# Optimization experiments

Measured on AMD Instinct MI355X. Metric: run time of the kernel, lower is better.

Reference implementation:

```python
import jax, jax.numpy as jnp
import numpy as np

N_BINS = 15
N, C = 1000000, 128


def setup_inputs() -> dict:
    key = jax.random.key(0)
    k1, k2 = jax.random.split(key)
    logits = jax.random.normal(k1, (N, C), dtype=jnp.float32)
    labels = jax.random.randint(k2, (N,), 0, C, dtype=jnp.int32)
    return {"logits": logits, "labels": labels}


def reference(logits, labels):
    # softmax + confidence/prediction (single pass, no [N,C] score re-materialization beyond probs)
    probs = jax.nn.softmax(logits, axis=1)            # [N, C]
    conf = jnp.max(probs, axis=1)                     # [N]
    pred = jnp.argmax(probs, axis=1)                  # [N]
    acc = (pred == labels).astype(conf.dtype)         # [N]

    # bin i covers (i/n_bins, (i+1)/n_bins]; searchsorted(uppers, conf, 'left')
    # gives the smallest j with uppers[j] >= conf, i.e. conf <= upper and conf > lower
    uppers = jnp.linspace(0.0, 1.0, N_BINS + 1, dtype=conf.dtype)[1:]  # [n_bins]
    bin_idx = jnp.clip(jnp.searchsorted(uppers, conf, side="left"), 0, N_BINS - 1)

    # fused histogram / segment reduce replacing the per-bin python loop
    counts = jax.ops.segment_sum(jnp.ones_like(conf), bin_idx, num_segments=N_BINS)
    sum_conf = jax.ops.segment_sum(conf, bin_idx, num_segments=N_BINS)
    sum_acc = jax.ops.segment_sum(acc, bin_idx, num_segments=N_BINS)

    nonempty = counts > 0
    safe = jnp.where(nonempty, counts, jnp.ones_like(counts))
    avg_conf = sum_conf / safe                        # per-bin avg confidence
    avg_acc = sum_acc / safe                          # per-bin accuracy

    gap = jnp.abs(avg_conf - avg_acc)
    # max over non-empty bins only (original skips bins with prop_in_bin == 0)
    mce = jnp.max(jnp.where(nonempty, gap, -jnp.inf))

    prob = jnp.where(nonempty, avg_conf, jnp.zeros_like(avg_conf))
    accu = jnp.where(nonempty, avg_acc, jnp.zeros_like(avg_acc))
    return mce, prob, accu
```

## Files before the change

### kernel.cpp

```cpp
#include <hip/hip_runtime.h>

#define NBINS 15

__global__ __launch_bounds__(256) void mce_pass1(
    const float* __restrict__ logits, const int* __restrict__ labels,
    unsigned long long* __restrict__ conf_part,
    unsigned int* __restrict__ cnt_part,
    unsigned int* __restrict__ acc_part,
    int n)
{
    __shared__ unsigned int s_cnt[NBINS];
    __shared__ unsigned int s_acc[NBINS];
    __shared__ unsigned long long s_conf[NBINS];
    if (threadIdx.x < NBINS) {
        s_cnt[threadIdx.x] = 0u;
        s_acc[threadIdx.x] = 0u;
        s_conf[threadIdx.x] = 0ULL;
    }
    __syncthreads();

    const int lane32 = threadIdx.x & 31;
    const int half   = (threadIdx.x >> 5) & 1;
    const int hw_global = blockIdx.x * 8 + (threadIdx.x >> 5);
    const int hw_total = gridDim.x * 8;

    for (int row = hw_global; row < n; row += hw_total) {
        const float4 v = *(const float4*)(logits + (size_t)row * 128 + lane32 * 4);
        const int lab = labels[row];

        float m4 = fmaxf(fmaxf(v.x, v.y), fmaxf(v.z, v.w));

        float M = m4;
        #pragma unroll
        for (int off = 16; off >= 1; off >>= 1)
            M = fmaxf(M, __shfl_xor(M, off, 32));

        int idx_local = (v.x == M) ? 0 : (v.y == M) ? 1 : (v.z == M) ? 2 : 3;
        unsigned long long bal = __ballot(m4 == M);
        unsigned int mask32 = (unsigned int)(bal >> (half << 5));
        int win_lane = __ffs(mask32) - 1;
        int win_local = __shfl(idx_local, win_lane, 32);
        int pred = (win_lane << 2) + win_local;

        float s = __expf(v.x - M) + __expf(v.y - M) + __expf(v.z - M) + __expf(v.w - M);
        #pragma unroll
        for (int off = 16; off >= 1; off >>= 1)
            s += __shfl_xor(s, off, 32);

        if (lane32 == 0) {
            float conf = 1.0f / s;
            int bin = (int)ceilf(conf * 15.0f) - 1;
            bin = max(0, min(NBINS - 1, bin));
            unsigned int acc = (pred == lab) ? 1u : 0u;
            unsigned long long fc = (unsigned long long)((double)conf * 4294967296.0);
            atomicAdd(&s_cnt[bin], 1u);
            atomicAdd(&s_acc[bin], acc);
            atomicAdd(&s_conf[bin], fc);
        }
    }
    __syncthreads();
    if (threadIdx.x < NBINS) {
        cnt_part[blockIdx.x * NBINS + threadIdx.x]  = s_cnt[threadIdx.x];
        acc_part[blockIdx.x * NBINS + threadIdx.x]  = s_acc[threadIdx.x];
        conf_part[blockIdx.x * NBINS + threadIdx.x] = s_conf[threadIdx.x];
    }
}

__global__ __launch_bounds__(960) void mce_pass2(
    const unsigned long long* __restrict__ conf_part,
    const unsigned int* __restrict__ cnt_part,
    const unsigned int* __restrict__ acc_part,
    int B, float* __restrict__ out)
{
    __shared__ float s_prob[NBINS], s_accu[NBINS], s_gap[NBINS];
    __shared__ int s_ne[NBINS];

    const int bin  = threadIdx.x >> 6;
    const int lane = threadIdx.x & 63;

    unsigned long long csum = 0ULL;
    unsigned int cn = 0u, ac = 0u;
    for (int i = lane; i < B; i += 64) {
        csum += conf_part[i * NBINS + bin];
        cn   += cnt_part[i * NBINS + bin];
        ac   += acc_part[i * NBINS + bin];
    }
    #pragma unroll
    for (int off = 32; off >= 1; off >>= 1) {
        csum += __shfl_xor(csum, off, 64);
        cn   += __shfl_xor(cn, off, 64);
        ac   += __shfl_xor(ac, off, 64);
    }

    if (lane == 0) {
        if (cn > 0u) {
            float p = (float)(((double)csum * (1.0 / 4294967296.0)) / (double)cn);
            float a = (float)((double)ac / (double)cn);
            s_prob[bin] = p;
            s_accu[bin] = a;
            s_gap[bin]  = fabsf(p - a);
            s_ne[bin]   = 1;
        } else {
            s_prob[bin] = 0.0f;
            s_accu[bin] = 0.0f;
            s_gap[bin]  = 0.0f;
            s_ne[bin]   = 0;
        }
    }
    __syncthreads();

    if (threadIdx.x == 0) {
        float mce = -1e30f;
        for (int b = 0; b < NBINS; ++b)
            if (s_ne[b] && s_gap[b] > mce) mce = s_gap[b];
        out[0] = mce;
    }
    if (threadIdx.x < NBINS) {
        out[1 + threadIdx.x]  = s_prob[threadIdx.x];
        out[16 + threadIdx.x] = s_accu[threadIdx.x];
    }
}

extern "C" void kernel_launch(void* const* d_in, const int* in_sizes, int n_in,
                              void* d_out, int out_size, void* d_ws, size_t ws_size,
                              hipStream_t stream) {
    const float* logits = (const float*)d_in[0];
    const int*   labels = (const int*)d_in[1];
    const int n = in_sizes[1];

    int B = 2048;
    const size_t per_block = (size_t)NBINS * (8 + 4 + 4);
    if ((size_t)B * per_block > ws_size) B = (int)(ws_size / per_block);
    if (B < 1) B = 1;

    unsigned long long* conf_part = (unsigned long long*)d_ws;
    unsigned int* cnt_part = (unsigned int*)((char*)d_ws + (size_t)B * NBINS * 8);
    unsigned int* acc_part = (unsigned int*)((char*)d_ws + (size_t)B * NBINS * 12);

    mce_pass1<<<B, 256, 0, stream>>>(logits, labels, conf_part, cnt_part, acc_part, n);
    mce_pass2<<<1, 960, 0, stream>>>(conf_part, cnt_part, acc_part, B, (float*)d_out);
}
```

Measured before the change: 665.9 us.

## Use DPP row reductions with readlane broadcast and transpose partial-histogram layout

Replaces the per-half-wave shuffle-xor max and sum reductions with DPP-based row/half reductions, then broadcasts results via readlane from lanes 31/63. The argmax winner lookup now uses readlane instead of a shuffle, and the double-precision fixed-point conversion of confidence becomes an integer mantissa shift. Partial histograms are stored bin-major so the second pass reads them coalesced, and the first pass gains an occupancy hint. The kernel is likely memory-bound on a 512MB read, so the ALU savings may matter little. The DPP control sequence must be correct for 32-lane halves.

New measurement: 664.5 us. About the same (-0.2%).

```diff
diff --git a/kernel.cpp b/kernel.cpp
--- a/kernel.cpp
+++ b/kernel.cpp
@@ -2,7 +2,30 @@
 
 #define NBINS 15
 
-__global__ __launch_bounds__(256) void mce_pass1(
+template <int CTRL>
+__device__ __forceinline__ float dpp_mov_f(float v) {
+    return __int_as_float(__builtin_amdgcn_update_dpp(
+        __float_as_int(v), __float_as_int(v), CTRL, 0xF, 0xF, false));
+}
+
+__device__ __forceinline__ float half_reduce_max(float v) {
+    v = fmaxf(v, dpp_mov_f<0xB1>(v));
+    v = fmaxf(v, dpp_mov_f<0x4E>(v));
+    v = fmaxf(v, dpp_mov_f<0x141>(v));
+    v = fmaxf(v, dpp_mov_f<0x140>(v));
+    v = fmaxf(v, dpp_mov_f<0x142>(v));
+    return v;
+}
+__device__ __forceinline__ float half_reduce_sum(float v) {
+    v += dpp_mov_f<0xB1>(v);
+    v += dpp_mov_f<0x4E>(v);
+    v += dpp_mov_f<0x141>(v);
+    v += dpp_mov_f<0x140>(v);
+    v += dpp_mov_f<0x142>(v);
+    return v;
+}
+
+__global__ __launch_bounds__(256, 8) void mce_pass1(
     const float* __restrict__ logits, const int* __restrict__ labels,
     unsigned long long* __restrict__ conf_part,
     unsigned int* __restrict__ cnt_part,
@@ -22,37 +45,46 @@
     const int lane32 = threadIdx.x & 31;
     const int half   = (threadIdx.x >> 5) & 1;
     const int hw_global = blockIdx.x * 8 + (threadIdx.x >> 5);
-    const int hw_total = gridDim.x * 8;
+    const int hw_total  = gridDim.x * 8;
+    const int B = gridDim.x;
 
     for (int row = hw_global; row < n; row += hw_total) {
         const float4 v = *(const float4*)(logits + (size_t)row * 128 + lane32 * 4);
         const int lab = labels[row];
 
         float m4 = fmaxf(fmaxf(v.x, v.y), fmaxf(v.z, v.w));
+        float Mr = half_reduce_max(m4);
+        const float MA = __int_as_float(__builtin_amdgcn_readlane(__float_as_int(Mr), 31));
+        const float MB = __int_as_float(__builtin_amdgcn_readlane(__float_as_int(Mr), 63));
+        const float Mh = half ? MB : MA;
 
-        float M = m4;
-        #pragma unroll
-        for (int off = 16; off >= 1; off >>= 1)
-            M = fmaxf(M, __shfl_xor(M, off, 32));
+        float e = __expf(v.x - Mh) + __expf(v.y - Mh) + __expf(v.z - Mh) + __expf(v.w - Mh);
+        float Sr = half_reduce_sum(e);
+        const int SA = __builtin_amdgcn_readlane(__float_as_int(Sr), 31);
+        const int SB = __builtin_amdgcn_readlane(__float_as_int(Sr), 63);
 
-        int idx_local = (v.x == M) ? 0 : (v.y == M) ? 1 : (v.z == M) ? 2 : 3;
-        unsigned long long bal = __ballot(m4 == M);
-        unsigned int mask32 = (unsigned int)(bal >> (half << 5));
-        int win_lane = __ffs(mask32) - 1;
-        int win_local = __shfl(idx_local, win_lane, 32);
-        int pred = (win_lane << 2) + win_local;
-
-        float s = __expf(v.x - M) + __expf(v.y - M) + __expf(v.z - M) + __expf(v.w - M);
-        #pragma unroll
-        for (int off = 16; off >= 1; off >>= 1)
-            s += __shfl_xor(s, off, 32);
+        int idx_local = (v.x == Mh) ? 0 : (v.y == Mh) ? 1 : (v.z == Mh) ? 2 : 3;
+        unsigned long long bal = __ballot(m4 == Mh);
+        unsigned lo = (unsigned)bal;
+        unsigned hi = (unsigned)(bal >> 32);
+        int winA = __ffs(lo) - 1;
+        int winB = __ffs(hi) - 1;
+        int predA = (winA << 2) + __builtin_amdgcn_readlane(idx_local, winA);
+        int predB = (winB << 2) + __builtin_amdgcn_readlane(idx_local, winB + 32);
 
         if (lane32 == 0) {
-            float conf = 1.0f / s;
+            float Sh = __int_as_float(half ? SB : SA);
+            int pred = half ? predB : predA;
+            float conf = 1.0f / Sh;
             int bin = (int)ceilf(conf * 15.0f) - 1;
             bin = max(0, min(NBINS - 1, bin));
             unsigned int acc = (pred == lab) ? 1u : 0u;
-            unsigned long long fc = (unsigned long long)((double)conf * 4294967296.0);
+            unsigned int cb = __float_as_uint(conf);
+            unsigned int mant = (cb & 0x7fffffu) | 0x800000u;
+            int sh = (int)(cb >> 23) - 118;
+            unsigned long long fc = (sh >= 0)
+                ? ((unsigned long long)mant << sh)
+                : ((unsigned long long)mant >> (-sh));
             atomicAdd(&s_cnt[bin], 1u);
             atomicAdd(&s_acc[bin], acc);
             atomicAdd(&s_conf[bin], fc);
@@ -60,9 +92,9 @@
     }
     __syncthreads();
     if (threadIdx.x < NBINS) {
-        cnt_part[blockIdx.x * NBINS + threadIdx.x]  = s_cnt[threadIdx.x];
-        acc_part[blockIdx.x * NBINS + threadIdx.x]  = s_acc[threadIdx.x];
-        conf_part[blockIdx.x * NBINS + threadIdx.x] = s_conf[threadIdx.x];
+        cnt_part[threadIdx.x * B + blockIdx.x]  = s_cnt[threadIdx.x];
+        acc_part[threadIdx.x * B + blockIdx.x]  = s_acc[threadIdx.x];
+        conf_part[(size_t)threadIdx.x * B + blockIdx.x] = s_conf[threadIdx.x];
     }
 }
 
@@ -80,10 +112,11 @@
 
     unsigned long long csum = 0ULL;
     unsigned int cn = 0u, ac = 0u;
+    #pragma unroll 4
     for (int i = lane; i < B; i += 64) {
-        csum += conf_part[i * NBINS + bin];
-        cn   += cnt_part[i * NBINS + bin];
-        ac   += acc_part[i * NBINS + bin];
+        csum += conf_part[(size_t)bin * B + i];
+        cn   += cnt_part[bin * B + i];
+        ac   += acc_part[bin * B + i];
     }
     #pragma unroll
     for (int off = 32; off >= 1; off >>= 1) {
```
